# Optimization experiments

Measured on AMD Instinct MI355X. Metric: run time of the kernel, lower is better.

The kernel has to match this reference:

```python
import jax, jax.numpy as jnp
import numpy as np

BINS = 16
EDGE_KS = 11
EDGE_SIGMA = 1.5
EPS = 1e-9


def _gauss1d(ks, sigma):
    x = jnp.arange(ks, dtype=jnp.float32) - (ks - 1) / 2.0
    g = jnp.exp(-(x * x) / (2.0 * sigma * sigma))
    return g / jnp.sum(g)


def _conv2d(x, k):
    # x: [B,Cin,H,W], k: [Cout,Cin,kh,kw], VALID padding
    return jax.lax.conv_general_dilated(x, k, (1, 1), 'VALID',
                                        dimension_numbers=('NCHW', 'OIHW', 'NCHW'))


def _gaussian_blur(x, ks, sigma):
    g = _gauss1d(ks, sigma)
    k = jnp.outer(g, g)[None, None]  # [1,1,ks,ks]
    p = ks // 2
    xp = jnp.pad(x, ((0, 0), (0, 0), (p, p), (p, p)), mode='reflect')
    return _conv2d(xp, k)


# 8 neighbor offsets ordered by angle 0,45,...,315 (kornia canny convention)
_OFFS = [(0, 1), (1, 1), (1, 0), (1, -1), (0, -1), (-1, -1), (-1, 0), (-1, 1)]


def _dir_kernels(center, nbr):
    ks = np.zeros((8, 1, 3, 3), np.float32)
    for i, (dy, dx) in enumerate(_OFFS):
        ks[i, 0, 1, 1] = center
        ks[i, 0, 1 + dy, 1 + dx] = nbr
    return jnp.asarray(ks)


NMS_K = _dir_kernels(1.0, -1.0)   # center minus directional neighbor
HYST_K = _dir_kernels(0.0, 1.0)   # directional neighbor value
SOBEL = jnp.asarray(np.stack([
    np.array([[-1, 0, 1], [-2, 0, 2], [-1, 0, 1]], np.float32),
    np.array([[-1, -2, -1], [0, 0, 0], [1, 2, 1]], np.float32)])[:, None])  # [2,1,3,3]


def _canny_edges(gray, low=0.1, high=0.2):
    blurred = _gaussian_blur(gray, 5, 1.0)
    gp = jnp.pad(blurred, ((0, 0), (0, 0), (1, 1), (1, 1)), mode='edge')
    grads = _conv2d(gp, SOBEL)                       # [B,2,H,W]
    gx, gy = grads[:, :1], grads[:, 1:]
    mag = jnp.sqrt(gx * gx + gy * gy + 1e-6)
    ang = jnp.round(jnp.rad2deg(jnp.arctan2(gy, gx)) / 45.0)
    pos_i = jnp.mod(ang, 8).astype(jnp.int32)        # [B,1,H,W]
    neg_i = jnp.mod(ang + 4, 8).astype(jnp.int32)
    mp = jnp.pad(mag, ((0, 0), (0, 0), (1, 1), (1, 1)))
    nms = _conv2d(mp, NMS_K)                         # [B,8,H,W]
    pos = jnp.take_along_axis(nms, pos_i, axis=1)
    neg = jnp.take_along_axis(nms, neg_i, axis=1)
    mag = mag * (jnp.minimum(pos, neg) > 0.0)
    edges = (mag > low).astype(jnp.float32) * 0.5 + (mag > high).astype(jnp.float32) * 0.5

    def body(c):
        e, _ = c
        weak = (e == 0.5).astype(jnp.float32)
        strong = (e == 1.0).astype(jnp.float32)
        nb = _conv2d(jnp.pad(e, ((0, 0), (0, 0), (1, 1), (1, 1))), HYST_K)
        hm = jnp.any(nb == 1.0, axis=1, keepdims=True).astype(jnp.float32) * weak + strong
        return (hm + (hm == 0.0) * weak * 0.5, e)

    def cond(c):
        e, old = c
        return jnp.any(e != old)

    edges, _ = jax.lax.while_loop(cond, body, (edges, -jnp.ones_like(edges)))
    return (edges == 1.0).astype(jnp.float32)


def _normalize_map(m):
    B = m.shape[0]
    f = m.reshape(B, -1)
    mn = f.min(axis=1).reshape(B, 1, 1, 1)
    mx = f.max(axis=1).reshape(B, 1, 1, 1)
    return (m - mn) / (mx - mn + EPS)


def _srd(x_norm, mean, std, alpha, beta):
    B, C, H, W = x_norm.shape
    x = jnp.clip(x_norm * std + mean, 0.0, 1.0)
    gray = 0.299 * x[:, :1] + 0.587 * x[:, 1:2] + 0.114 * x[:, 2:3]
    edges = _canny_edges(gray)
    edge_density = _gaussian_blur(edges, EDGE_KS, EDGE_SIGMA)
    # per-image color histogram sparsity, batched via offset indices
    qc = jnp.round(x * (BINS - 1)).astype(jnp.int32)
    combined = qc[:, 0] * BINS * BINS + qc[:, 1] * BINS + qc[:, 2]   # [B,H,W]
    nbins = BINS ** 3
    flat = combined.reshape(B, -1) + (jnp.arange(B, dtype=jnp.int32) * nbins)[:, None]
    counts = jnp.zeros(B * nbins, jnp.float32).at[flat.reshape(-1)].add(1.0)
    probs = counts / float(H * W)
    sparsity = -jnp.log(probs[flat] + EPS).reshape(B, 1, H, W)
    fused = alpha * _normalize_map(edge_density) + beta * _normalize_map(sparsity)
    return jax.nn.sigmoid(fused)


def setup_inputs():
    key = jax.random.key(0)
    x_norm = jax.random.normal(key, (16, 3, 512, 512), jnp.float32)
    mean = jnp.array([0.485, 0.456, 0.406], jnp.float32).reshape(1, 3, 1, 1)
    std = jnp.array([0.229, 0.224, 0.225], jnp.float32).reshape(1, 3, 1, 1)
    return {'x_norm': x_norm, 'mean': mean, 'std': std,
            'alpha': jnp.float32(1.0), 'beta': jnp.float32(1.0)}


def reference(x_norm, mean, std, alpha, beta):
    return _srd(x_norm, mean, std, alpha, beta)
```

## Files before the change

kernel.cpp:

```cpp
#include <hip/hip_runtime.h>
#include <stdint.h>

#define NB 16
#define HH 512
#define WW 512
#define HW (HH*WW)
#define NBINS 4096

typedef unsigned long long u64;

__device__ __forceinline__ float clip01(float v){ return fminf(fmaxf(v, 0.0f), 1.0f); }
__device__ __forceinline__ int refl(int i, int n){ if (i < 0) i = -i; if (i >= n) i = 2*n - 2 - i; return i; }
__device__ __forceinline__ int clampi(int i, int lo, int hi){ return i < lo ? lo : (i > hi ? hi : i); }

__global__ void __launch_bounds__(256) k_canny(const float* __restrict__ x,
                                               const float* __restrict__ mean,
                                               const float* __restrict__ stdv,
                                               u64* __restrict__ A, u64* __restrict__ Sb,
                                               uint4* __restrict__ hist4)
{
#pragma clang fp contract(off)
  __shared__ float ubuf[40*73];
  __shared__ float blr[36*69];
  __shared__ uint8_t sdir[32*64];
  int b = blockIdx.x;
  int img = b >> 7;
  int t = b & 127;
  int y0 = (t >> 3) << 5;
  int x0 = (t & 7) << 6;
  int tid = threadIdx.x;
  if (tid < 8) hist4[b*8 + tid] = make_uint4(0u,0u,0u,0u);
  float g5[5]; { float s=0.0f; for(int i=0;i<5;i++){ float tt=(float)i-2.0f; g5[i]=expf(-(tt*tt)/2.0f); s+=g5[i]; } for(int i=0;i<5;i++) g5[i]/=s; }
  float m0 = mean[0], m1 = mean[1], m2 = mean[2];
  float s0 = stdv[0], s1 = stdv[1], s2 = stdv[2];
  const float* xb = x + (size_t)img * 3 * HW;
  for (int i = tid; i < 40*72; i += 256){
    int ly = i/72, lx = i - ly*72;
    int gy = refl(y0 - 4 + ly, HH);
    int gx = refl(x0 - 4 + lx, WW);
    int p = gy*WW + gx;
    float cr = clip01(xb[p]        *s0 + m0);
    float cg = clip01(xb[HW + p]   *s1 + m1);
    float cbv= clip01(xb[2*HW + p] *s2 + m2);
    ubuf[ly*73 + lx] = 0.299f*cr + 0.587f*cg + 0.114f*cbv;
  }
  __syncthreads();
  for (int task = tid; task < 272; task += 256){
    int lx = task % 68;
    int ly = (task / 68) * 9;
    float w[5][5];
    #pragma unroll
    for (int j = 0; j < 4; j++)
      #pragma unroll
      for (int k = 0; k < 5; k++)
        w[j][k] = ubuf[(ly+j)*73 + lx + k];
    #pragma unroll
    for (int s = 0; s < 9; s++){
      #pragma unroll
      for (int k = 0; k < 5; k++) w[4][k] = ubuf[(ly+s+4)*73 + lx + k];
      float acc = 0.0f;
      #pragma unroll
      for (int ky = 0; ky < 5; ky++)
        #pragma unroll
        for (int kx = 0; kx < 5; kx++)
          acc += (g5[ky]*g5[kx]) * w[ky][kx];
      blr[(ly+s)*69 + lx] = acc;
      #pragma unroll
      for (int j = 0; j < 4; j++)
        #pragma unroll
        for (int k = 0; k < 5; k++) w[j][k] = w[j+1][k];
    }
  }
  __syncthreads();
  for (int i = tid; i < 34*66; i += 256){
    int ly = i/66, lx = i - ly*66;
    int Y = y0 - 1 + ly, X = x0 - 1 + lx;
    float m = 0.0f;
    if (Y >= 0 && Y < HH && X >= 0 && X < WW){
      float v[3][3];
      for (int dy = 0; dy < 3; dy++){
        int Yl = clampi(Y + dy - 1, 0, HH-1) - (y0 - 2);
        for (int dx = 0; dx < 3; dx++){
          int Xl = clampi(X + dx - 1, 0, WW-1) - (x0 - 2);
          v[dy][dx] = blr[Yl*69 + Xl];
        }
      }
      float gx = (v[0][2] - v[0][0]) + 2.0f*(v[1][2] - v[1][0]) + (v[2][2] - v[2][0]);
      float gy = (v[2][0] + 2.0f*v[2][1] + v[2][2]) - (v[0][0] + 2.0f*v[0][1] + v[0][2]);
      m = sqrtf(gx*gx + gy*gy + 1e-6f);
      if (ly >= 1 && ly <= 32 && lx >= 1 && lx <= 64){
        float ax = fabsf(gx), ay = fabsf(gy);
        int d;
        if (ay <= 0.41421356237309503f*ax) d = (gx >= 0.0f) ? 0 : 4;
        else if (ay >= 2.4142135623730951f*ax) d = (gy > 0.0f) ? 2 : 6;
        else if (gx > 0.0f) d = (gy > 0.0f) ? 1 : 7;
        else d = (gy > 0.0f) ? 3 : 5;
        sdir[(ly-1)*64 + (lx-1)] = (uint8_t)d;
      }
    }
    ubuf[ly*67 + lx] = m;
  }
  __syncthreads();
  const int OY[8] = {0,1,1,1,0,-1,-1,-1};
  const int OX[8] = {1,1,0,-1,-1,-1,0,1};
  int lane = tid & 63, wv = tid >> 6;
  for (int j = 0; j < 8; j++){
    int y = j*4 + wv;
    int xx0 = lane;
    float m = ubuf[(y+1)*67 + (xx0+1)];
    int d  = sdir[y*64 + xx0];
    int d2 = (d + 4) & 7;
    float mp = 0.0f, mn = 0.0f;
    { int yy=y+OY[d],  xx=xx0+OX[d];  int gy=y0+yy, gx=x0+xx; if(gy>=0&&gy<HH&&gx>=0&&gx<WW) mp = ubuf[(yy+1)*67 + (xx+1)]; }
    { int yy=y+OY[d2], xx=xx0+OX[d2]; int gy=y0+yy, gx=x0+xx; if(gy>=0&&gy<HH&&gx>=0&&gx<WW) mn = ubuf[(yy+1)*67 + (xx+1)]; }
    bool keep = ((m - mp) > 0.0f) && ((m - mn) > 0.0f);
    float mf = keep ? m : 0.0f;
    bool strong = mf > 0.2f;
    bool weak   = (mf > 0.1f) && !strong;
    u64 wb = __ballot(weak);
    u64 sb = __ballot(strong);
    if (lane == 0){
      int gy = y0 + y;
      A [img*4096 + gy*8 + (x0>>6)] = wb;
      Sb[img*4096 + gy*8 + (x0>>6)] = sb;
    }
  }
}

__device__ __forceinline__ u64 ks_flood(u64 g, u64 P){
  u64 p1 = P, g1 = g;
  g1 |= p1 & (g1 << 1);  p1 &= (p1 << 1);
  g1 |= p1 & (g1 << 2);  p1 &= (p1 << 2);
  g1 |= p1 & (g1 << 4);  p1 &= (p1 << 4);
  g1 |= p1 & (g1 << 8);  p1 &= (p1 << 8);
  g1 |= p1 & (g1 << 16); p1 &= (p1 << 16);
  g1 |= p1 & (g1 << 32);
  u64 p2 = P, g2 = g;
  g2 |= p2 & (g2 >> 1);  p2 &= (p2 >> 1);
  g2 |= p2 & (g2 >> 2);  p2 &= (p2 >> 2);
  g2 |= p2 & (g2 >> 4);  p2 &= (p2 >> 4);
  g2 |= p2 & (g2 >> 8);  p2 &= (p2 >> 8);
  g2 |= p2 & (g2 >> 16); p2 &= (p2 >> 16);
  g2 |= p2 & (g2 >> 32);
  return g1 | g2;
}

#define HROW(m, l, r_) ((m) | ((m)<<1) | ((m)>>1) | ((l)>>63) | ((r_)<<63))

#define UPD(i) do{ \
    u64 pend = Pr[i] & ~Sr[i]; \
    if (pend){ \
      u64 Sv = Sr[i]; \
      int r = r0 + (i); \
      u64 mu = ((i) > 0) ? Sr[(i)-1] : (r > 0   ? sS[(r-1)*9+w] : 0ull); \
      u64 md = ((i) < 7) ? Sr[(i)+1] : (r < 511 ? sS[(r+1)*9+w] : 0ull); \
      u64 lu = (left  && r > 0)   ? sS[(r-1)*9+w-1] : 0ull; \
      u64 ru = (right && r > 0)   ? sS[(r-1)*9+w+1] : 0ull; \
      u64 lm = left  ? sS[r*9+w-1] : 0ull; \
      u64 rm = right ? sS[r*9+w+1] : 0ull; \
      u64 ldn= (left  && r < 511) ? sS[(r+1)*9+w-1] : 0ull; \
      u64 rdn= (right && r < 511) ? sS[(r+1)*9+w+1] : 0ull; \
      u64 nb = HROW(mu,lu,ru) | HROW(Sv,lm,rm) | HROW(md,ldn,rdn); \
      u64 g = Sv | (Pr[i] & nb); \
      if (g != Sv){ \
        u64 ns = ks_flood(g, Pr[i]); \
        Sr[i] = ns; sS[r*9+w] = ns; changed = true; \
      } \
    } \
  } while(0)

__global__ void __launch_bounds__(512) k_mid(const u64* __restrict__ A, u64* __restrict__ S,
                                             const float* __restrict__ x,
                                             const float* __restrict__ mean,
                                             const float* __restrict__ stdv,
                                             uint16_t* __restrict__ comb,
                                             uint32_t* __restrict__ hist)
{
#pragma clang fp contract(off)
  __shared__ __align__(16) char smem[512*9*8];
  int tid = threadIdx.x;
  if (blockIdx.x < 16){
    u64* sS = (u64*)smem;
    int img = blockIdx.x;
    const u64* gA = A + img * 4096;
    u64*       gS = S + img * 4096;
    for (int i = tid; i < 4096; i += 512)
      sS[(i>>3)*9 + (i&7)] = gS[i];
    __syncthreads();
    int  w     = tid & 7;
    int  r0    = (tid >> 3) << 3;
    bool left  = (w > 0), right = (w < 7);
    u64 Sr[8], Pr[8];
    #pragma unroll
    for (int i = 0; i < 8; i++){
      Sr[i] = sS[(r0+i)*9 + w];
      Pr[i] = gA[(r0+i)*8 + w] | Sr[i];
    }
    for (;;){
      bool changed = false;
      #pragma unroll 1
      for (int rep = 0; rep < 2; rep++){
        #pragma unroll
        for (int i = 0; i < 8; i++) UPD(i);
        #pragma unroll
        for (int i = 7; i >= 0; i--) UPD(i);
      }
      if (!__syncthreads_or(changed ? 1 : 0)) break;
    }
    #pragma unroll
    for (int i = 0; i < 8; i++) gS[(r0+i)*8 + w] = Sr[i];
  } else {
    uint32_t* h = (uint32_t*)smem;
    int pb  = blockIdx.x - 16;
    int img = pb >> 5;
    int base = (pb & 31) * 8192;
    for (int i = tid; i < NBINS; i += 512) h[i] = 0u;
    __syncthreads();
    float m0 = mean[0], m1 = mean[1], m2 = mean[2];
    float s0 = stdv[0], s1 = stdv[1], s2 = stdv[2];
    const float* xb = x + (size_t)img * 3 * HW;
    uint16_t*  cb   = comb + (size_t)img*HW;
    #pragma unroll
    for (int it = 0; it < 4; it++){
      int f4 = it*512 + tid;
      int p  = base + f4*4;
      float4 r = *(const float4*)(xb + p);
      float4 g = *(const float4*)(xb + HW + p);
      float4 b = *(const float4*)(xb + 2*HW + p);
      float xr[4] = {r.x, r.y, r.z, r.w};
      float xg[4] = {g.x, g.y, g.z, g.w};
      float xbl[4] = {b.x, b.y, b.z, b.w};
      uint16_t cc[4];
      #pragma unroll
      for (int j = 0; j < 4; j++){
        float cr = clip01(xr[j]*s0 + m0);
        float cg = clip01(xg[j]*s1 + m1);
        float cbv= clip01(xbl[j]*s2 + m2);
        int c = ((int)rintf(cr*15.0f))*256 + ((int)rintf(cg*15.0f))*16 + (int)rintf(cbv*15.0f);
        cc[j] = (uint16_t)c;
        atomicAdd(&h[c], 1u);
      }
      ushort4 cv; cv.x = cc[0]; cv.y = cc[1]; cv.z = cc[2]; cv.w = cc[3];
      *(ushort4*)(cb + p) = cv;
    }
    __syncthreads();
    uint32_t* gh = hist + img * NBINS;
    for (int i = tid; i < NBINS; i += 512){ uint32_t v = h[i]; if (v) atomicAdd(&gh[i], v); }
  }
}

__global__ void __launch_bounds__(256) k_b11(const u64* __restrict__ S, float* __restrict__ out,
                                             float2* __restrict__ part)
{
#pragma clang fp contract(off)
  __shared__ u64 wds[74][3];
  __shared__ float hb[74][64];
  __shared__ float smn[4], smx[4];
  int b = blockIdx.x;
  int img = b >> 6;
  int t = b & 63;
  int y0 = (t >> 3) << 6;
  int tx = t & 7;
  int x0 = tx << 6;
  int tid = threadIdx.x;
  float g[11]; { float s=0.0f; for(int i=0;i<11;i++){ float tt=(float)i-5.0f; g[i]=expf(-(tt*tt)/4.5f); s+=g[i]; } for(int i=0;i<11;i++) g[i]/=s; }
  for (int i = tid; i < 74*3; i += 256){
    int j = i/3, widx = i - j*3;
    int gy = refl(y0 - 5 + j, HH);
    int gw = tx - 1 + widx;
    wds[j][widx] = (gw >= 0 && gw < 8) ? S[img*4096 + gy*8 + gw] : 0ull;
  }
  __syncthreads();
  for (int i = tid; i < 74*64; i += 256){
    int j = i >> 6, c = i & 63;
    float acc = 0.0f;
    for (int k = 0; k < 11; k++){
      int xx = refl(x0 + c + k - 5, WW);
      int widx = (xx >> 6) - tx + 1;
      float bv = (float)((wds[j][widx] >> (xx & 63)) & 1ull);
      acc += g[k] * bv;
    }
    hb[j][c] = acc;
  }
  __syncthreads();
  float mn = 3.4e38f, mx = -3.4e38f;
  float* ob = out + (size_t)img*HW;
  for (int i = tid; i < 4096; i += 256){
    int y = i >> 6, c = i & 63;
    float acc = 0.0f;
    for (int k = 0; k < 11; k++) acc += g[k] * hb[y + k][c];
    ob[(y0 + y)*WW + x0 + c] = acc;
    mn = fminf(mn, acc); mx = fmaxf(mx, acc);
  }
  for (int off = 32; off >= 1; off >>= 1){
    mn = fminf(mn, __shfl_down(mn, off));
    mx = fmaxf(mx, __shfl_down(mx, off));
  }
  int wv = tid >> 6, ln = tid & 63;
  if (ln == 0){ smn[wv] = mn; smx[wv] = mx; }
  __syncthreads();
  if (tid == 0){
    part[b] = make_float2(fminf(fminf(smn[0],smn[1]),fminf(smn[2],smn[3])),
                          fmaxf(fmaxf(smx[0],smx[1]),fmaxf(smx[2],smx[3])));
  }
}

__global__ void __launch_bounds__(256) k_edred(const float2* __restrict__ part,
                                               const uint32_t* __restrict__ hist,
                                               uint32_t* __restrict__ stats){
  __shared__ uint32_t sx[4], sn[4];
  int img = blockIdx.x;
  int tid = threadIdx.x;
  uint32_t mx = 0u, mn = 0xFFFFFFFFu;
  for (int i = tid; i < NBINS; i += 256){
    uint32_t c = hist[img*NBINS + i];
    if (c > mx) mx = c;
    if (c > 0u && c < mn) mn = c;
  }
  for (int off = 32; off >= 1; off >>= 1){
    uint32_t ox = (uint32_t)__shfl_down((int)mx, off);
    uint32_t on = (uint32_t)__shfl_down((int)mn, off);
    if (ox > mx) mx = ox;
    if (on < mn) mn = on;
  }
  int wv = tid >> 6, ln = tid & 63;
  if (ln == 0){ sx[wv] = mx; sn[wv] = mn; }
  float fmn = 3.4e38f, fmx = -3.4e38f;
  if (wv == 0){
    float2 v = part[img*64 + ln];
    fmn = v.x; fmx = v.y;
    for (int off = 32; off >= 1; off >>= 1){
      fmn = fminf(fmn, __shfl_down(fmn, off));
      fmx = fmaxf(fmx, __shfl_down(fmx, off));
    }
  }
  __syncthreads();
  if (tid == 0){
    uint32_t MX = max(max(sx[0],sx[1]), max(sx[2],sx[3]));
    uint32_t MN = min(min(sn[0],sn[1]), min(sn[2],sn[3]));
    stats[img*4+0] = __float_as_uint(fmn);
    stats[img*4+1] = __float_as_uint(fmx);
    stats[img*4+2] = __float_as_uint(-logf((float)MX / 262144.0f + 1e-9f));
    stats[img*4+3] = __float_as_uint(-logf((float)MN / 262144.0f + 1e-9f));
  }
}

__global__ void k_final(const float* __restrict__ ed, const uint16_t* __restrict__ comb,
                        const uint32_t* __restrict__ hist, const uint32_t* __restrict__ stats,
                        const float* __restrict__ alpha, const float* __restrict__ beta,
                        float* __restrict__ out)
{
#pragma clang fp contract(off)
  int idx = blockIdx.x * 256 + threadIdx.x;
  int img = idx >> 18;
  float a = alpha[0], b = beta[0];
  float mne = __uint_as_float(stats[img*4+0]);
  float mxe = __uint_as_float(stats[img*4+1]);
  float mns = __uint_as_float(stats[img*4+2]);
  float mxs = __uint_as_float(stats[img*4+3]);
  float e  = ed[idx];
  float sp = -logf((float)hist[img*NBINS + comb[idx]] / 262144.0f + 1e-9f);
  float en = (e  - mne) / (mxe - mne + 1e-9f);
  float sn = (sp - mns) / (mxs - mns + 1e-9f);
  float f  = a*en + b*sn;
  out[idx] = 1.0f / (1.0f + expf(-f));
}

extern "C" void kernel_launch(void* const* d_in, const int* in_sizes, int n_in,
                              void* d_out, int out_size, void* d_ws, size_t ws_size,
                              hipStream_t stream)
{
  const float* x     = (const float*)d_in[0];
  const float* mean  = (const float*)d_in[1];
  const float* stdv  = (const float*)d_in[2];
  const float* alpha = (const float*)d_in[3];
  const float* beta  = (const float*)d_in[4];
  float* out = (float*)d_out;

  char* ws = (char*)d_ws;
  uint16_t* comb  = (uint16_t*)ws;
  float2*   part  = (float2*)(ws + (8u << 20));
  uint32_t* hist  = (uint32_t*)(ws + (9u << 20));
  u64*      Ab    = (u64*)(ws + (10u << 20));
  u64*      Sb    = (u64*)(ws + (11u << 20));
  uint32_t* stats = (uint32_t*)(ws + (12u << 20));

  hipLaunchKernelGGL(k_canny, dim3(2048),  dim3(256), 0, stream, x, mean, stdv, Ab, Sb, (uint4*)hist);
  hipLaunchKernelGGL(k_mid,   dim3(528),   dim3(512), 0, stream, Ab, Sb, x, mean, stdv, comb, hist);
  hipLaunchKernelGGL(k_b11,   dim3(1024),  dim3(256), 0, stream, Sb, out, part);
  hipLaunchKernelGGL(k_edred, dim3(NB),    dim3(256), 0, stream, part, hist, stats);
  hipLaunchKernelGGL(k_final, dim3(16384), dim3(256), 0, stream, out, comb, hist, stats, alpha, beta, out);
}
```

Measured before the change: 127.8 us.

## Split grayscale and color quantization into a dedicated pass before canny

Adds a k_gray kernel that reads the RGB input once with vectorized loads, writes a float grayscale plane and the quantized color index map, and zeroes the histogram. k_canny now loads the precomputed grayscale halo instead of recomputing it from three channels, and the histogram blocks in k_mid read 16-bit indices instead of the float input. This cuts redundant 3-channel reads and arithmetic on the halos, at the cost of an extra launch and a 16 MB gray plane written and read back.

```diff
diff --git a/kernel.cpp b/kernel.cpp
--- a/kernel.cpp
+++ b/kernel.cpp
@@ -13,11 +13,51 @@
 __device__ __forceinline__ int refl(int i, int n){ if (i < 0) i = -i; if (i >= n) i = 2*n - 2 - i; return i; }
 __device__ __forceinline__ int clampi(int i, int lo, int hi){ return i < lo ? lo : (i > hi ? hi : i); }
 
-__global__ void __launch_bounds__(256) k_canny(const float* __restrict__ x,
-                                               const float* __restrict__ mean,
-                                               const float* __restrict__ stdv,
-                                               u64* __restrict__ A, u64* __restrict__ Sb,
-                                               uint4* __restrict__ hist4)
+__global__ void __launch_bounds__(256) k_gray(const float* __restrict__ x,
+                                              const float* __restrict__ mean,
+                                              const float* __restrict__ stdv,
+                                              float* __restrict__ gray,
+                                              uint16_t* __restrict__ comb,
+                                              uint4* __restrict__ hist4)
+{
+#pragma clang fp contract(off)
+  int b = blockIdx.x, tid = threadIdx.x;
+  if (b < 64) hist4[b*256 + tid] = make_uint4(0u,0u,0u,0u);
+  int img  = b >> 6;
+  int base = (b & 63) * 4096;
+  float m0 = mean[0], m1 = mean[1], m2 = mean[2];
+  float s0 = stdv[0], s1 = stdv[1], s2 = stdv[2];
+  const float* xb = x + (size_t)img * 3 * HW;
+  float*     gb   = gray + (size_t)img*HW;
+  uint16_t*  cb   = comb + (size_t)img*HW;
+  #pragma unroll
+  for (int it = 0; it < 4; it++){
+    int f4 = it*256 + tid;
+    int p  = base + f4*4;
+    float4 r = *(const float4*)(xb + p);
+    float4 g = *(const float4*)(xb + HW + p);
+    float4 bl= *(const float4*)(xb + 2*HW + p);
+    float xr[4] = {r.x, r.y, r.z, r.w};
+    float xg[4] = {g.x, g.y, g.z, g.w};
+    float xbl[4] = {bl.x, bl.y, bl.z, bl.w};
+    float gy[4]; uint16_t cc[4];
+    #pragma unroll
+    for (int j = 0; j < 4; j++){
+      float cr = clip01(xr[j]*s0 + m0);
+      float cg = clip01(xg[j]*s1 + m1);
+      float cbv= clip01(xbl[j]*s2 + m2);
+      gy[j] = 0.299f*cr + 0.587f*cg + 0.114f*cbv;
+      int c = ((int)rintf(cr*15.0f))*256 + ((int)rintf(cg*15.0f))*16 + (int)rintf(cbv*15.0f);
+      cc[j] = (uint16_t)c;
+    }
+    *(float4*)(gb + p) = make_float4(gy[0], gy[1], gy[2], gy[3]);
+    ushort4 cv; cv.x = cc[0]; cv.y = cc[1]; cv.z = cc[2]; cv.w = cc[3];
+    *(ushort4*)(cb + p) = cv;
+  }
+}
+
+__global__ void __launch_bounds__(256) k_canny(const float* __restrict__ gray,
+                                               u64* __restrict__ A, u64* __restrict__ Sb)
 {
 #pragma clang fp contract(off)
   __shared__ float ubuf[40*73];
@@ -28,21 +68,14 @@
   int t = b & 127;
   int y0 = (t >> 3) << 5;
   int x0 = (t & 7) << 6;
+  const float* gb = gray + (size_t)img*HW;
   int tid = threadIdx.x;
-  if (tid < 8) hist4[b*8 + tid] = make_uint4(0u,0u,0u,0u);
   float g5[5]; { float s=0.0f; for(int i=0;i<5;i++){ float tt=(float)i-2.0f; g5[i]=expf(-(tt*tt)/2.0f); s+=g5[i]; } for(int i=0;i<5;i++) g5[i]/=s; }
-  float m0 = mean[0], m1 = mean[1], m2 = mean[2];
-  float s0 = stdv[0], s1 = stdv[1], s2 = stdv[2];
-  const float* xb = x + (size_t)img * 3 * HW;
   for (int i = tid; i < 40*72; i += 256){
     int ly = i/72, lx = i - ly*72;
     int gy = refl(y0 - 4 + ly, HH);
     int gx = refl(x0 - 4 + lx, WW);
-    int p = gy*WW + gx;
-    float cr = clip01(xb[p]        *s0 + m0);
-    float cg = clip01(xb[HW + p]   *s1 + m1);
-    float cbv= clip01(xb[2*HW + p] *s2 + m2);
-    ubuf[ly*73 + lx] = 0.299f*cr + 0.587f*cg + 0.114f*cbv;
+    ubuf[ly*73 + lx] = gb[gy*WW + gx];
   }
   __syncthreads();
   for (int task = tid; task < 272; task += 256){
@@ -170,13 +203,9 @@
   } while(0)
 
 __global__ void __launch_bounds__(512) k_mid(const u64* __restrict__ A, u64* __restrict__ S,
-                                             const float* __restrict__ x,
-                                             const float* __restrict__ mean,
-                                             const float* __restrict__ stdv,
-                                             uint16_t* __restrict__ comb,
+                                             const uint16_t* __restrict__ comb,
                                              uint32_t* __restrict__ hist)
 {
-#pragma clang fp contract(off)
   __shared__ __align__(16) char smem[512*9*8];
   int tid = threadIdx.x;
   if (blockIdx.x < 16){
@@ -216,32 +245,15 @@
     int base = (pb & 31) * 8192;
     for (int i = tid; i < NBINS; i += 512) h[i] = 0u;
     __syncthreads();
-    float m0 = mean[0], m1 = mean[1], m2 = mean[2];
-    float s0 = stdv[0], s1 = stdv[1], s2 = stdv[2];
-    const float* xb = x + (size_t)img * 3 * HW;
-    uint16_t*  cb   = comb + (size_t)img*HW;
+    const uint16_t* cb = comb + (size_t)img*HW;
     #pragma unroll
     for (int it = 0; it < 4; it++){
       int f4 = it*512 + tid;
-      int p  = base + f4*4;
-      float4 r = *(const float4*)(xb + p);
-      float4 g = *(const float4*)(xb + HW + p);
-      float4 b = *(const float4*)(xb + 2*HW + p);
-      float xr[4] = {r.x, r.y, r.z, r.w};
-      float xg[4] = {g.x, g.y, g.z, g.w};
-      float xbl[4] = {b.x, b.y, b.z, b.w};
-      uint16_t cc[4];
-      #pragma unroll
-      for (int j = 0; j < 4; j++){
-        float cr = clip01(xr[j]*s0 + m0);
-        float cg = clip01(xg[j]*s1 + m1);
-        float cbv= clip01(xbl[j]*s2 + m2);
-        int c = ((int)rintf(cr*15.0f))*256 + ((int)rintf(cg*15.0f))*16 + (int)rintf(cbv*15.0f);
-        cc[j] = (uint16_t)c;
-        atomicAdd(&h[c], 1u);
-      }
-      ushort4 cv; cv.x = cc[0]; cv.y = cc[1]; cv.z = cc[2]; cv.w = cc[3];
-      *(ushort4*)(cb + p) = cv;
+      ushort4 cv = *(const ushort4*)(cb + base + f4*4);
+      atomicAdd(&h[cv.x], 1u);
+      atomicAdd(&h[cv.y], 1u);
+      atomicAdd(&h[cv.z], 1u);
+      atomicAdd(&h[cv.w], 1u);
     }
     __syncthreads();
     uint32_t* gh = hist + img * NBINS;
@@ -378,15 +390,17 @@
   float* out = (float*)d_out;
 
   char* ws = (char*)d_ws;
-  uint16_t* comb  = (uint16_t*)ws;
-  float2*   part  = (float2*)(ws + (8u << 20));
-  uint32_t* hist  = (uint32_t*)(ws + (9u << 20));
-  u64*      Ab    = (u64*)(ws + (10u << 20));
-  u64*      Sb    = (u64*)(ws + (11u << 20));
-  uint32_t* stats = (uint32_t*)(ws + (12u << 20));
-
-  hipLaunchKernelGGL(k_canny, dim3(2048),  dim3(256), 0, stream, x, mean, stdv, Ab, Sb, (uint4*)hist);
-  hipLaunchKernelGGL(k_mid,   dim3(528),   dim3(512), 0, stream, Ab, Sb, x, mean, stdv, comb, hist);
+  float*    gray  = (float*)ws;
+  uint16_t* comb  = (uint16_t*)(ws + (16u << 20));
+  float2*   part  = (float2*)(ws + (24u << 20));
+  uint32_t* hist  = (uint32_t*)(ws + (25u << 20));
+  u64*      Ab    = (u64*)(ws + (26u << 20));
+  u64*      Sb    = (u64*)(ws + (27u << 20));
+  uint32_t* stats = (uint32_t*)(ws + (28u << 20));
+
+  hipLaunchKernelGGL(k_gray,  dim3(1024),  dim3(256), 0, stream, x, mean, stdv, gray, comb, (uint4*)hist);
+  hipLaunchKernelGGL(k_canny, dim3(2048),  dim3(256), 0, stream, gray, Ab, Sb);
+  hipLaunchKernelGGL(k_mid,   dim3(528),   dim3(512), 0, stream, Ab, Sb, comb, hist);
   hipLaunchKernelGGL(k_b11,   dim3(1024),  dim3(256), 0, stream, Sb, out, part);
   hipLaunchKernelGGL(k_edred, dim3(NB),    dim3(256), 0, stream, part, hist, stats);
   hipLaunchKernelGGL(k_final, dim3(16384), dim3(256), 0, stream, out, comb, hist, stats, alpha, beta, out);
```

Result: slower. 131.2 us (+2.7%).
